# Optimization experiments

Measured on AMD Instinct MI355X. Metric: run time of the kernel, lower is better.

The kernel has to match this reference:

```python
import jax, jax.numpy as jnp
import numpy as np

QB = 127.0  # 2**(8-1) - 1


def ternary_dequant(w):
    # absmean ternary quantization, then dequantize by scale
    scale = jnp.mean(jnp.abs(w))
    w_t = jnp.clip(jnp.round(w / (scale + 1e-8)), -1.0, 1.0)
    w_t = jnp.where(scale == 0.0, jnp.zeros_like(w), w_t)
    return w_t * scale


def activation_quantize(x):
    # per-row (last-dim) absmax int8 fake-quant
    scale = jnp.max(jnp.abs(x), axis=-1, keepdims=True) / QB
    scale = jnp.maximum(scale, 1e-8)
    return jnp.clip(jnp.round(x / scale), -QB, QB) * scale


def setup_inputs() -> dict:
    key = jax.random.key(0)
    kx, kw = jax.random.split(key)
    x = jax.random.normal(kx, (2, 4096, 4096), dtype=jnp.float32)
    # kaiming_uniform-ish init scale; exact init distribution is irrelevant to the math
    bound = 1.0 / np.sqrt(4096)
    weight = jax.random.uniform(kw, (4096, 4096), dtype=jnp.float32,
                                minval=-bound, maxval=bound)
    return {"x": x, "weight": weight}


def reference(x, weight):
    w_q = ternary_dequant(weight)        # [out, in]
    x_q = activation_quantize(x)         # [b, s, in]
    return jnp.einsum('bsi,oi->bso', x_q, w_q)
```

## Files before the change

### kernel.cpp

```cpp
#include <hip/hip_runtime.h>
#include <stdint.h>
#include <stddef.h>


#define K_DIM 4096
#define M_DIM 8192
#define N_DIM 4096

typedef int v4i __attribute__((ext_vector_type(4)));

__device__ __forceinline__ void async_copy16(void* lds, const void* g) {
  __builtin_amdgcn_global_load_lds(
      (const __attribute__((address_space(1))) unsigned int*)g,
      (__attribute__((address_space(3))) unsigned int*)lds,
      16, 0, 0);
}

__global__ void k_wsum(const float* __restrict__ w, double* __restrict__ partials) {
  const float4* w4 = (const float4*)w;
  int tid = blockIdx.x * 256 + threadIdx.x;
  double s = 0.0;
  for (int i = tid; i < 4194304; i += 262144) {
    float4 v = w4[i];
    s += (double)fabsf(v.x) + (double)fabsf(v.y) +
         (double)fabsf(v.z) + (double)fabsf(v.w);
  }
  for (int off = 32; off > 0; off >>= 1) s += __shfl_down(s, off);
  __shared__ double lsum[4];
  int lane = threadIdx.x & 63, wid = threadIdx.x >> 6;
  if (lane == 0) lsum[wid] = s;
  __syncthreads();
  if (threadIdx.x == 0)
    partials[blockIdx.x] = lsum[0] + lsum[1] + lsum[2] + lsum[3];
}

__global__ void k_wscale(const double* __restrict__ partials, float* __restrict__ wscale) {
  double s = 0.0;
  for (int i = threadIdx.x; i < 1024; i += 256) s += partials[i];
  for (int off = 32; off > 0; off >>= 1) s += __shfl_down(s, off);
  __shared__ double lsum[4];
  int lane = threadIdx.x & 63, wid = threadIdx.x >> 6;
  if (lane == 0) lsum[wid] = s;
  __syncthreads();
  if (threadIdx.x == 0) {
    double tot = lsum[0] + lsum[1] + lsum[2] + lsum[3];
    *wscale = (float)(tot / 16777216.0);
  }
}

__global__ void k_wq(const float* __restrict__ w, const float* __restrict__ wscale,
                     char* __restrict__ qw) {
  float d = *wscale + 1e-8f;
  const float4* w4 = (const float4*)w;
  int* q4 = (int*)qw;
  int tid = blockIdx.x * 256 + threadIdx.x;
  for (int i = tid; i < 4194304; i += 524288) {
    float4 v = w4[i];
    int a = (int)fmaxf(fminf(rintf(v.x / d), 1.f), -1.f);
    int b = (int)fmaxf(fminf(rintf(v.y / d), 1.f), -1.f);
    int c = (int)fmaxf(fminf(rintf(v.z / d), 1.f), -1.f);
    int e = (int)fmaxf(fminf(rintf(v.w / d), 1.f), -1.f);
    q4[i] = (a & 255) | ((b & 255) << 8) | ((c & 255) << 16) | ((e & 255) << 24);
  }
}

__global__ void k_xq(const float* __restrict__ x, char* __restrict__ qx,
                     float* __restrict__ sx) {
  int row = blockIdx.x;
  const float4* xr = (const float4*)(x + (size_t)row * K_DIM);
  float4 v[4];
  float m = 0.f;
#pragma unroll
  for (int c = 0; c < 4; c++) {
    v[c] = xr[threadIdx.x + c * 256];
    m = fmaxf(m, fmaxf(fmaxf(fabsf(v[c].x), fabsf(v[c].y)),
                       fmaxf(fabsf(v[c].z), fabsf(v[c].w))));
  }
  for (int off = 32; off > 0; off >>= 1) m = fmaxf(m, __shfl_down(m, off));
  __shared__ float lm[4];
  __shared__ float bscale;
  int lane = threadIdx.x & 63, wid = threadIdx.x >> 6;
  if (lane == 0) lm[wid] = m;
  __syncthreads();
  if (threadIdx.x == 0) {
    float mm = fmaxf(fmaxf(lm[0], lm[1]), fmaxf(lm[2], lm[3]));
    float sc = fmaxf(mm / 127.0f, 1e-8f);
    bscale = sc;
    sx[row] = sc;
  }
  __syncthreads();
  float sc = bscale;
  int* q4 = (int*)(qx + (size_t)row * K_DIM);
#pragma unroll
  for (int c = 0; c < 4; c++) {
    int a = (int)fmaxf(fminf(rintf(v[c].x / sc), 127.f), -127.f);
    int b = (int)fmaxf(fminf(rintf(v[c].y / sc), 127.f), -127.f);
    int cc = (int)fmaxf(fminf(rintf(v[c].z / sc), 127.f), -127.f);
    int e = (int)fmaxf(fminf(rintf(v[c].w / sc), 127.f), -127.f);
    q4[threadIdx.x + c * 256] = (a & 255) | ((b & 255) << 8) | ((cc & 255) << 16) | ((e & 255) << 24);
  }
}

__global__ void k_gemm(const char* __restrict__ qx, const char* __restrict__ qw,
                       const float* __restrict__ sx, const float* __restrict__ wscale,
                       float* __restrict__ out) {
  __shared__ char ldsA[128 * 64];
  __shared__ char ldsB[128 * 64];

  const int bn = blockIdx.x & 31;
  const int bm = blockIdx.x >> 5;
  const int rowBase = bm * 128;
  const int colBase = bn * 128;
  const int tid = threadIdx.x;
  const int lane = tid & 63;
  const int wave = tid >> 6;
  const int wr = wave >> 1, wc = wave & 1;

  v4i acc[4][4] = {};

  const int sRow = wave * 32 + (lane >> 2);
  const int sK = (lane & 3) * 16;
  const char* gA0 = qx + (size_t)(rowBase + sRow) * K_DIM + sK;
  const char* gA1 = gA0 + 16 * K_DIM;
  const char* gB0 = qw + (size_t)(colBase + sRow) * K_DIM + sK;
  const char* gB1 = gB0 + 16 * K_DIM;
  char* lA0 = ldsA + wave * 2048;
  char* lA1 = lA0 + 1024;
  char* lB0 = ldsB + wave * 2048;
  char* lB1 = lB0 + 1024;

  const int kseg = (lane >> 4) * 16;
  const char* aPtr = ldsA + (wr * 64 + (lane & 15)) * 64 + kseg;
  const char* bPtr = ldsB + (wc * 64 + (lane & 15)) * 64 + kseg;

  for (int kb = 0; kb < K_DIM / 64; kb++) {
    if (kb) __syncthreads();
    const int goff = kb * 64;
    async_copy16(lA0, gA0 + goff);
    async_copy16(lA1, gA1 + goff);
    async_copy16(lB0, gB0 + goff);
    async_copy16(lB1, gB1 + goff);
    __syncthreads();

    v4i a[4], b[4];
#pragma unroll
    for (int t = 0; t < 4; t++) {
      a[t] = *(const v4i*)(aPtr + t * 16 * 64);
      b[t] = *(const v4i*)(bPtr + t * 16 * 64);
    }
#pragma unroll
    for (int mt = 0; mt < 4; mt++)
#pragma unroll
      for (int nt = 0; nt < 4; nt++)
        acc[mt][nt] = __builtin_amdgcn_mfma_i32_16x16x64_i8(a[mt], b[nt], acc[mt][nt], 0, 0, 0);
  }

  const float sw = *wscale;
  const int col0 = colBase + wc * 64 + (lane & 15);
  const int row0 = rowBase + wr * 64 + (lane >> 4) * 4;
#pragma unroll
  for (int mt = 0; mt < 4; mt++) {
#pragma unroll
    for (int r = 0; r < 4; r++) {
      const int row = row0 + mt * 16 + r;
      const float s = sx[row] * sw;
#pragma unroll
      for (int nt = 0; nt < 4; nt++)
        out[(size_t)row * N_DIM + col0 + nt * 16] = (float)acc[mt][nt][r] * s;
    }
  }
}

extern "C" void kernel_launch(void* const* d_in, const int* in_sizes, int n_in,
                              void* d_out, int out_size, void* d_ws, size_t ws_size,
                              hipStream_t stream) {
  const float* x = (const float*)d_in[0];
  const float* w = (const float*)d_in[1];
  float* out = (float*)d_out;
  char* ws = (char*)d_ws;

  double* partials = (double*)ws;
  float* wscale    = (float*)(ws + 8192);
  float* sx        = (float*)(ws + 8448);
  char*  qw        = ws + 41472;
  char*  qx        = ws + 41472 + 16777216;

  k_wsum  <<<1024, 256, 0, stream>>>(w, partials);
  k_wscale<<<   1, 256, 0, stream>>>(partials, wscale);
  k_wq    <<<2048, 256, 0, stream>>>(w, wscale, qw);
  k_xq    <<<8192, 256, 0, stream>>>(x, qx, sx);
  k_gemm  <<<64 * 32, 256, 0, stream>>>(qx, qw, sx, wscale, out);
}
```

Baseline: 419.1 us.

## Store GEMM LDS tiles in MFMA fragment order and fuse weight-scale reduction

Reorders the global-to-LDS async copies so each lane's 16-byte MFMA operand fragment is stored contiguously, making LDS reads a linear lane*16 pattern instead of a 64-byte strided one. This is meant to remove bank conflicts. It also folds the single-block weight-scale reduction into the weight-quantize kernel, with every block redundantly reducing the partials, to drop one launch. Activation quantization now multiplies by a reciprocal instead of dividing, which can change rounding in edge cases.

```diff
diff --git a/kernel.cpp b/kernel.cpp
--- a/kernel.cpp
+++ b/kernel.cpp
@@ -34,23 +34,24 @@
     partials[blockIdx.x] = lsum[0] + lsum[1] + lsum[2] + lsum[3];
 }
 
-__global__ void k_wscale(const double* __restrict__ partials, float* __restrict__ wscale) {
+__global__ void k_wq(const float* __restrict__ w, const double* __restrict__ partials,
+                     float* __restrict__ wscale, char* __restrict__ qw) {
   double s = 0.0;
   for (int i = threadIdx.x; i < 1024; i += 256) s += partials[i];
   for (int off = 32; off > 0; off >>= 1) s += __shfl_down(s, off);
   __shared__ double lsum[4];
+  __shared__ float bsc;
   int lane = threadIdx.x & 63, wid = threadIdx.x >> 6;
   if (lane == 0) lsum[wid] = s;
   __syncthreads();
   if (threadIdx.x == 0) {
     double tot = lsum[0] + lsum[1] + lsum[2] + lsum[3];
-    *wscale = (float)(tot / 16777216.0);
+    float sc = (float)(tot / 16777216.0);
+    bsc = sc;
+    if (blockIdx.x == 0) *wscale = sc;
   }
-}
-
-__global__ void k_wq(const float* __restrict__ w, const float* __restrict__ wscale,
-                     char* __restrict__ qw) {
-  float d = *wscale + 1e-8f;
+  __syncthreads();
+  float d = bsc + 1e-8f;
   const float4* w4 = (const float4*)w;
   int* q4 = (int*)qw;
   int tid = blockIdx.x * 256 + threadIdx.x;
@@ -89,14 +90,14 @@
     sx[row] = sc;
   }
   __syncthreads();
-  float sc = bscale;
+  float inv = 1.0f / bscale;
   int* q4 = (int*)(qx + (size_t)row * K_DIM);
 #pragma unroll
   for (int c = 0; c < 4; c++) {
-    int a = (int)fmaxf(fminf(rintf(v[c].x / sc), 127.f), -127.f);
-    int b = (int)fmaxf(fminf(rintf(v[c].y / sc), 127.f), -127.f);
-    int cc = (int)fmaxf(fminf(rintf(v[c].z / sc), 127.f), -127.f);
-    int e = (int)fmaxf(fminf(rintf(v[c].w / sc), 127.f), -127.f);
+    int a = (int)fmaxf(fminf(rintf(v[c].x * inv), 127.f), -127.f);
+    int b = (int)fmaxf(fminf(rintf(v[c].y * inv), 127.f), -127.f);
+    int cc = (int)fmaxf(fminf(rintf(v[c].z * inv), 127.f), -127.f);
+    int e = (int)fmaxf(fminf(rintf(v[c].w * inv), 127.f), -127.f);
     q4[threadIdx.x + c * 256] = (a & 255) | ((b & 255) << 8) | ((cc & 255) << 16) | ((e & 255) << 24);
   }
 }
@@ -104,8 +105,8 @@
 __global__ void k_gemm(const char* __restrict__ qx, const char* __restrict__ qw,
                        const float* __restrict__ sx, const float* __restrict__ wscale,
                        float* __restrict__ out) {
-  __shared__ char ldsA[128 * 64];
-  __shared__ char ldsB[128 * 64];
+  __shared__ char ldsA[8192];
+  __shared__ char ldsB[8192];
 
   const int bn = blockIdx.x & 31;
   const int bm = blockIdx.x >> 5;
@@ -118,20 +119,19 @@
 
   v4i acc[4][4] = {};
 
-  const int sRow = wave * 32 + (lane >> 2);
-  const int sK = (lane & 3) * 16;
-  const char* gA0 = qx + (size_t)(rowBase + sRow) * K_DIM + sK;
+  const int fr = lane & 15;
+  const int fk = (lane >> 4) * 16;
+  const char* gA0 = qx + (size_t)(rowBase + wave * 32 + fr) * K_DIM + fk;
   const char* gA1 = gA0 + 16 * K_DIM;
-  const char* gB0 = qw + (size_t)(colBase + sRow) * K_DIM + sK;
+  const char* gB0 = qw + (size_t)(colBase + wave * 32 + fr) * K_DIM + fk;
   const char* gB1 = gB0 + 16 * K_DIM;
   char* lA0 = ldsA + wave * 2048;
   char* lA1 = lA0 + 1024;
   char* lB0 = ldsB + wave * 2048;
   char* lB1 = lB0 + 1024;
 
-  const int kseg = (lane >> 4) * 16;
-  const char* aPtr = ldsA + (wr * 64 + (lane & 15)) * 64 + kseg;
-  const char* bPtr = ldsB + (wc * 64 + (lane & 15)) * 64 + kseg;
+  const char* aBase = ldsA + wr * 4096 + lane * 16;
+  const char* bBase = ldsB + wc * 4096 + lane * 16;
 
   for (int kb = 0; kb < K_DIM / 64; kb++) {
     if (kb) __syncthreads();
@@ -145,8 +145,8 @@
     v4i a[4], b[4];
 #pragma unroll
     for (int t = 0; t < 4; t++) {
-      a[t] = *(const v4i*)(aPtr + t * 16 * 64);
-      b[t] = *(const v4i*)(bPtr + t * 16 * 64);
+      a[t] = *(const v4i*)(aBase + t * 1024);
+      b[t] = *(const v4i*)(bBase + t * 1024);
     }
 #pragma unroll
     for (int mt = 0; mt < 4; mt++)
@@ -185,9 +185,8 @@
   char*  qw        = ws + 41472;
   char*  qx        = ws + 41472 + 16777216;
 
-  k_wsum  <<<1024, 256, 0, stream>>>(w, partials);
-  k_wscale<<<   1, 256, 0, stream>>>(partials, wscale);
-  k_wq    <<<2048, 256, 0, stream>>>(w, wscale, qw);
-  k_xq    <<<8192, 256, 0, stream>>>(x, qx, sx);
-  k_gemm  <<<64 * 32, 256, 0, stream>>>(qx, qw, sx, wscale, out);
+  k_wsum <<<1024, 256, 0, stream>>>(w, partials);
+  k_wq   <<<2048, 256, 0, stream>>>(w, partials, wscale, qw);
+  k_xq   <<<8192, 256, 0, stream>>>(x, qx, sx);
+  k_gemm <<<64 * 32, 256, 0, stream>>>(qx, qw, sx, wscale, out);
 }
```

Measured after the change: 511.9 us. 1.22x slower.
